# Performance work log

Measured on AMD Instinct MI355X. Metric: run time of the kernel, lower is better.

The kernel has to match this reference:

```python
import jax, jax.numpy as jnp
import numpy as np

N_CHANNELS = 64
# Static leave-one-out index table: row c lists all channels != c. Shape [C, C-1].
_LOO_IDX = np.array([[j for j in range(N_CHANNELS) if j != c] for c in range(N_CHANNELS)], dtype=np.int32)


def setup_inputs() -> dict:
    key = jax.random.key(0)
    kx, kw = jax.random.split(key)
    B, S, C = 4, 8192, N_CHANNELS
    x = jax.random.normal(kx, (B, S, C, 2), dtype=jnp.float32)
    # Stacked weights of the C Linear(2*(C-1) -> 2, bias=False) layers: [C, 2, 2*(C-1)].
    fan_in = 2 * (C - 1)
    bound = 1.0 / np.sqrt(fan_in)
    W = jax.random.uniform(kw, (C, 2, fan_in), dtype=jnp.float32, minval=-bound, maxval=bound)
    return {"x": x, "W": W}


def reference(x, W):
    # x: [B, S, C, 2] (real/imag), W: [C, 2, 2*(C-1)]
    idx = jnp.asarray(_LOO_IDX)                      # [C, C-1]
    amp = x[..., 0] ** 2 + x[..., 1] ** 2            # [B, S, C]
    distorted = amp[..., None] * x                   # [B, S, C, 2]
    fr = distorted[..., 0]                           # [B, S, C]
    fi = distorted[..., 1]                           # [B, S, C]
    # Leave-one-out gather for every target channel c: [B, S, C, C-1]
    fr_loo = fr[..., idx]
    fi_loo = fi[..., idx]
    total = jnp.concatenate([fr_loo, fi_loo], axis=-1)  # [B, S, C, 2*(C-1)]
    # Per-channel tiny linear, batched across B, S, C in one einsum.
    out = jnp.einsum('bscn,con->bsco', total, W)         # [B, S, C, 2]
    return out
```

## Files before the change

kernel.cpp:

```cpp
#include <hip/hip_runtime.h>


typedef _Float16 f16x8 __attribute__((ext_vector_type(8)));
typedef _Float16 f16x2 __attribute__((ext_vector_type(2)));
typedef float    floatx4 __attribute__((ext_vector_type(4)));

#define NPOS  32768
#define CPOS  64
#define NCH   2
#define BPOS  (CPOS * NCH)
#define NBLK  (NPOS / BPOS)
#define NTHR  512
#define MS    136

__global__ __launch_bounds__(NTHR, 2)
void leakage_kernel(const float* __restrict__ x,
                    const float* __restrict__ W,
                    float* __restrict__ out) {
    __shared__ __align__(16) _Float16 Mt[128][MS];
    __shared__ __align__(16) _Float16 fsh[CPOS][MS];

    const int tid  = threadIdx.x;
    const int w    = tid >> 6;
    const int lane = tid & 63;
    const int q    = lane >> 4, r = lane & 15;

    const float2* __restrict__ W2 = (const float2*)W;
#pragma unroll
    for (int it = 0; it < 16; ++it) {
        const int e  = tid + NTHR * it;
        const int n  = e >> 6;
        const int m2 = e & 63;
        if (m2 < 63) {
            const int c = n >> 1;
            const float2 v = W2[n * 63 + m2];
#pragma unroll
            for (int u = 0; u < 2; ++u) {
                const int m    = 2 * m2 + u;
                const int half = (m >= 63) ? 1 : 0;
                const int mh   = m - 63 * half;
                const int k    = 64 * half + mh + (mh >= c ? 1 : 0);
                Mt[n][k] = (_Float16)(u == 0 ? v.x : v.y);
            }
        }
    }
    if (tid < 128) {
        const int c = tid >> 1;
        Mt[tid][c]      = (_Float16)0.f;
        Mt[tid][64 + c] = (_Float16)0.f;
    }

    const int pblk = blockIdx.x * BPOS;

    {
        const float4* __restrict__ x4 = (const float4*)x + (size_t)pblk * 32;
#pragma unroll
        for (int it = 0; it < 4; ++it) {
            const int g = tid + NTHR * it;
            const int p = g >> 5;
            const int i = g & 31;
            const float4 v = x4[g];
            const float a0 = v.x * v.x + v.y * v.y;
            const float a1 = v.z * v.z + v.w * v.w;
            *(f16x2*)&fsh[p][2 * i] =
                f16x2{ (_Float16)(a0 * v.x), (_Float16)(a1 * v.z) };
            *(f16x2*)&fsh[p][64 + 2 * i] =
                f16x2{ (_Float16)(a0 * v.y), (_Float16)(a1 * v.w) };
        }
    }
    __syncthreads();

    f16x8 B0 = *(const f16x8*)&Mt[16 * w + r][ 0 + 8 * q];
    f16x8 B1 = *(const f16x8*)&Mt[16 * w + r][32 + 8 * q];
    f16x8 B2 = *(const f16x8*)&Mt[16 * w + r][64 + 8 * q];
    f16x8 B3 = *(const f16x8*)&Mt[16 * w + r][96 + 8 * q];

#pragma unroll
    for (int ch = 0; ch < NCH; ++ch) {
#pragma unroll
        for (int pt = 0; pt < 4; ++pt) {
            const int pr = pt * 16 + r;
            f16x8 A0 = *(const f16x8*)&fsh[pr][ 0 + 8 * q];
            f16x8 A1 = *(const f16x8*)&fsh[pr][32 + 8 * q];
            f16x8 A2 = *(const f16x8*)&fsh[pr][64 + 8 * q];
            f16x8 A3 = *(const f16x8*)&fsh[pr][96 + 8 * q];

            floatx4 C = {0.f, 0.f, 0.f, 0.f};
            C = __builtin_amdgcn_mfma_f32_16x16x32_f16(A0, B0, C, 0, 0, 0);
            C = __builtin_amdgcn_mfma_f32_16x16x32_f16(A1, B1, C, 0, 0, 0);
            C = __builtin_amdgcn_mfma_f32_16x16x32_f16(A2, B2, C, 0, 0, 0);
            C = __builtin_amdgcn_mfma_f32_16x16x32_f16(A3, B3, C, 0, 0, 0);

            float* __restrict__ op =
                out + (size_t)(pblk + ch * CPOS + pt * 16) * 128;
#pragma unroll
            for (int reg = 0; reg < 4; ++reg) {
                op[(size_t)(4 * q + reg) * 128 + 16 * w + r] = C[reg];
            }
        }

        if (ch + 1 < NCH) {
            __syncthreads();
            const float4* __restrict__ x4 =
                (const float4*)x + (size_t)(pblk + (ch + 1) * CPOS) * 32;
#pragma unroll
            for (int it = 0; it < 4; ++it) {
                const int g = tid + NTHR * it;
                const int p = g >> 5;
                const int i = g & 31;
                const float4 v = x4[g];
                const float a0 = v.x * v.x + v.y * v.y;
                const float a1 = v.z * v.z + v.w * v.w;
                *(f16x2*)&fsh[p][2 * i] =
                    f16x2{ (_Float16)(a0 * v.x), (_Float16)(a1 * v.z) };
                *(f16x2*)&fsh[p][64 + 2 * i] =
                    f16x2{ (_Float16)(a0 * v.y), (_Float16)(a1 * v.w) };
            }
            __syncthreads();
        }
    }
}

extern "C" void kernel_launch(void* const* d_in, const int* in_sizes, int n_in,
                              void* d_out, int out_size, void* d_ws, size_t ws_size,
                              hipStream_t stream) {
    const float* x = (const float*)d_in[0];
    const float* W = (const float*)d_in[1];
    float* out = (float*)d_out;

    hipLaunchKernelGGL(leakage_kernel, dim3(NBLK), dim3(NTHR), 0, stream,
                       x, W, out);
}
```

Before: 72.20 us.

## Double-buffer x chunks in LDS and prefetch loads ahead of compute

Global loads of the first x chunk are issued before the W-matrix setup, so their latency hides behind building the weight matrix in LDS. The second chunk is prefetched into registers before the first chunk's MFMA and store phase, and a second LDS buffer removes one of the block barriers. This trades extra registers and 17 KB more LDS per block for more overlap of memory latency with compute. The extra LDS may lower occupancy below the launch-bounds target of two blocks per CU.

```diff
diff --git a/kernel.cpp b/kernel.cpp
--- a/kernel.cpp
+++ b/kernel.cpp
@@ -7,23 +7,29 @@
 
 #define NPOS  32768
 #define CPOS  64
-#define NCH   2
-#define BPOS  (CPOS * NCH)
+#define BPOS  (CPOS * 2)
 #define NBLK  (NPOS / BPOS)
 #define NTHR  512
 #define MS    136
 
 __global__ __launch_bounds__(NTHR, 2)
-void leakage_kernel(const float* __restrict__ x,
-                    const float* __restrict__ W,
-                    float* __restrict__ out) {
+void leakage_kernel_pipe(const float* __restrict__ x,
+                         const float* __restrict__ W,
+                         float* __restrict__ out) {
     __shared__ __align__(16) _Float16 Mt[128][MS];
-    __shared__ __align__(16) _Float16 fsh[CPOS][MS];
+    __shared__ __align__(16) _Float16 fsh[2][CPOS][MS];
 
     const int tid  = threadIdx.x;
     const int w    = tid >> 6;
     const int lane = tid & 63;
     const int q    = lane >> 4, r = lane & 15;
+
+    const int pblk = blockIdx.x * BPOS;
+    const float4* __restrict__ x4 = (const float4*)x + (size_t)pblk * 32;
+
+    float4 v0[4];
+#pragma unroll
+    for (int it = 0; it < 4; ++it) v0[it] = x4[tid + NTHR * it];
 
     const float2* __restrict__ W2 = (const float2*)W;
 #pragma unroll
@@ -50,23 +56,18 @@
         Mt[tid][64 + c] = (_Float16)0.f;
     }
 
-    const int pblk = blockIdx.x * BPOS;
-
-    {
-        const float4* __restrict__ x4 = (const float4*)x + (size_t)pblk * 32;
 #pragma unroll
-        for (int it = 0; it < 4; ++it) {
-            const int g = tid + NTHR * it;
-            const int p = g >> 5;
-            const int i = g & 31;
-            const float4 v = x4[g];
-            const float a0 = v.x * v.x + v.y * v.y;
-            const float a1 = v.z * v.z + v.w * v.w;
-            *(f16x2*)&fsh[p][2 * i] =
-                f16x2{ (_Float16)(a0 * v.x), (_Float16)(a1 * v.z) };
-            *(f16x2*)&fsh[p][64 + 2 * i] =
-                f16x2{ (_Float16)(a0 * v.y), (_Float16)(a1 * v.w) };
-        }
+    for (int it = 0; it < 4; ++it) {
+        const int g = tid + NTHR * it;
+        const int p = g >> 5;
+        const int i = g & 31;
+        const float4 v = v0[it];
+        const float a0 = v.x * v.x + v.y * v.y;
+        const float a1 = v.z * v.z + v.w * v.w;
+        *(f16x2*)&fsh[0][p][2 * i] =
+            f16x2{ (_Float16)(a0 * v.x), (_Float16)(a1 * v.z) };
+        *(f16x2*)&fsh[0][p][64 + 2 * i] =
+            f16x2{ (_Float16)(a0 * v.y), (_Float16)(a1 * v.w) };
     }
     __syncthreads();
 
@@ -75,49 +76,64 @@
     f16x8 B2 = *(const f16x8*)&Mt[16 * w + r][64 + 8 * q];
     f16x8 B3 = *(const f16x8*)&Mt[16 * w + r][96 + 8 * q];
 
+    float4 v1[4];
 #pragma unroll
-    for (int ch = 0; ch < NCH; ++ch) {
+    for (int it = 0; it < 4; ++it) v1[it] = x4[2048 + tid + NTHR * it];
+
 #pragma unroll
-        for (int pt = 0; pt < 4; ++pt) {
-            const int pr = pt * 16 + r;
-            f16x8 A0 = *(const f16x8*)&fsh[pr][ 0 + 8 * q];
-            f16x8 A1 = *(const f16x8*)&fsh[pr][32 + 8 * q];
-            f16x8 A2 = *(const f16x8*)&fsh[pr][64 + 8 * q];
-            f16x8 A3 = *(const f16x8*)&fsh[pr][96 + 8 * q];
+    for (int pt = 0; pt < 4; ++pt) {
+        const int pr = pt * 16 + r;
+        f16x8 A0 = *(const f16x8*)&fsh[0][pr][ 0 + 8 * q];
+        f16x8 A1 = *(const f16x8*)&fsh[0][pr][32 + 8 * q];
+        f16x8 A2 = *(const f16x8*)&fsh[0][pr][64 + 8 * q];
+        f16x8 A3 = *(const f16x8*)&fsh[0][pr][96 + 8 * q];
 
-            floatx4 C = {0.f, 0.f, 0.f, 0.f};
-            C = __builtin_amdgcn_mfma_f32_16x16x32_f16(A0, B0, C, 0, 0, 0);
-            C = __builtin_amdgcn_mfma_f32_16x16x32_f16(A1, B1, C, 0, 0, 0);
-            C = __builtin_amdgcn_mfma_f32_16x16x32_f16(A2, B2, C, 0, 0, 0);
-            C = __builtin_amdgcn_mfma_f32_16x16x32_f16(A3, B3, C, 0, 0, 0);
+        floatx4 C = {0.f, 0.f, 0.f, 0.f};
+        C = __builtin_amdgcn_mfma_f32_16x16x32_f16(A0, B0, C, 0, 0, 0);
+        C = __builtin_amdgcn_mfma_f32_16x16x32_f16(A1, B1, C, 0, 0, 0);
+        C = __builtin_amdgcn_mfma_f32_16x16x32_f16(A2, B2, C, 0, 0, 0);
+        C = __builtin_amdgcn_mfma_f32_16x16x32_f16(A3, B3, C, 0, 0, 0);
 
-            float* __restrict__ op =
-                out + (size_t)(pblk + ch * CPOS + pt * 16) * 128;
+        float* __restrict__ op = out + (size_t)(pblk + pt * 16) * 128;
 #pragma unroll
-            for (int reg = 0; reg < 4; ++reg) {
-                op[(size_t)(4 * q + reg) * 128 + 16 * w + r] = C[reg];
-            }
-        }
+        for (int reg = 0; reg < 4; ++reg)
+            op[(size_t)(4 * q + reg) * 128 + 16 * w + r] = C[reg];
+    }
 
-        if (ch + 1 < NCH) {
-            __syncthreads();
-            const float4* __restrict__ x4 =
-                (const float4*)x + (size_t)(pblk + (ch + 1) * CPOS) * 32;
 #pragma unroll
-            for (int it = 0; it < 4; ++it) {
-                const int g = tid + NTHR * it;
-                const int p = g >> 5;
-                const int i = g & 31;
-                const float4 v = x4[g];
-                const float a0 = v.x * v.x + v.y * v.y;
-                const float a1 = v.z * v.z + v.w * v.w;
-                *(f16x2*)&fsh[p][2 * i] =
-                    f16x2{ (_Float16)(a0 * v.x), (_Float16)(a1 * v.z) };
-                *(f16x2*)&fsh[p][64 + 2 * i] =
-                    f16x2{ (_Float16)(a0 * v.y), (_Float16)(a1 * v.w) };
-            }
-            __syncthreads();
-        }
+    for (int it = 0; it < 4; ++it) {
+        const int g = tid + NTHR * it;
+        const int p = g >> 5;
+        const int i = g & 31;
+        const float4 v = v1[it];
+        const float a0 = v.x * v.x + v.y * v.y;
+        const float a1 = v.z * v.z + v.w * v.w;
+        *(f16x2*)&fsh[1][p][2 * i] =
+            f16x2{ (_Float16)(a0 * v.x), (_Float16)(a1 * v.z) };
+        *(f16x2*)&fsh[1][p][64 + 2 * i] =
+            f16x2{ (_Float16)(a0 * v.y), (_Float16)(a1 * v.w) };
+    }
+    __syncthreads();
+
+#pragma unroll
+    for (int pt = 0; pt < 4; ++pt) {
+        const int pr = pt * 16 + r;
+        f16x8 A0 = *(const f16x8*)&fsh[1][pr][ 0 + 8 * q];
+        f16x8 A1 = *(const f16x8*)&fsh[1][pr][32 + 8 * q];
+        f16x8 A2 = *(const f16x8*)&fsh[1][pr][64 + 8 * q];
+        f16x8 A3 = *(const f16x8*)&fsh[1][pr][96 + 8 * q];
+
+        floatx4 C = {0.f, 0.f, 0.f, 0.f};
+        C = __builtin_amdgcn_mfma_f32_16x16x32_f16(A0, B0, C, 0, 0, 0);
+        C = __builtin_amdgcn_mfma_f32_16x16x32_f16(A1, B1, C, 0, 0, 0);
+        C = __builtin_amdgcn_mfma_f32_16x16x32_f16(A2, B2, C, 0, 0, 0);
+        C = __builtin_amdgcn_mfma_f32_16x16x32_f16(A3, B3, C, 0, 0, 0);
+
+        float* __restrict__ op =
+            out + (size_t)(pblk + CPOS + pt * 16) * 128;
+#pragma unroll
+        for (int reg = 0; reg < 4; ++reg)
+            op[(size_t)(4 * q + reg) * 128 + 16 * w + r] = C[reg];
     }
 }
 
@@ -128,6 +144,6 @@
     const float* W = (const float*)d_in[1];
     float* out = (float*)d_out;
 
-    hipLaunchKernelGGL(leakage_kernel, dim3(NBLK), dim3(NTHR), 0, stream,
+    hipLaunchKernelGGL(leakage_kernel_pipe, dim3(NBLK), dim3(NTHR), 0, stream,
                        x, W, out);
 }
```

Result: no change. 71.01 us (-1.7%).
